# Performance work log

Measured on AMD Instinct MI355X. Metric: run time of the kernel, lower is better.

## Reference

```python
import jax, jax.numpy as jnp
import numpy as np

B = 8192; NP = 20; OBS = 17; ACT = 6; H = 256; N = B * NP
ACT_LIMIT = 1.0; SIGMA_P0 = 0.1; STEPS = 10; LR = 0.05
GAMMA = 1.0 / (1e-8 + 2.0 * 2.0 ** 2)  # kernel_sigma = 2.0
A0_TABLE = 5 * B * NP


def _q_net(x, W1, b1, W2, b2, W3, b3):
    h = jax.nn.relu(x @ W1 + b1)
    h = jax.nn.relu(h @ W2 + b2)
    return (h @ W3 + b3)[:, 0]


def _forward(obs, a0_table, q1_W1, q1_b1, q1_W2, q1_b2, q1_W3, q1_b3,
             q2_W1, q2_b1, q2_W2, q2_b2, q2_W3, q2_b3, idx):
    a0 = a0_table[idx]  # [N, ACT]
    eye = jnp.eye(NP, dtype=obs.dtype)

    def q_min(X):
        xi = jnp.concatenate([obs, X], axis=-1)
        return jnp.minimum(
            _q_net(xi, q1_W1, q1_b1, q1_W2, q1_b2, q1_W3, q1_b3),
            _q_net(xi, q2_W1, q2_b1, q2_W2, q2_b2, q2_W3, q2_b3))

    def step(carry, _):
        a, logp = carry
        logq, vjp_fn = jax.vjp(q_min, a)
        score = vjp_fn(jnp.ones_like(logq))[0]  # autograd.grad(log_prob.sum(), X)
        X = a.reshape(B, NP, ACT)
        S = score.reshape(B, NP, ACT)
        diff = X[:, :, None, :] - X[:, None, :, :]   # [B,n,n,d], x_i - x_j
        dist_sq = (diff ** 2).sum(-1)                # [B,n,n]
        K = jnp.exp(-GAMMA * dist_sq)                # K_XX
        K_grad = -2.0 * GAMMA * diff * K[..., None]  # grad_{x_i} K(x_i, x_j)
        phi = (jnp.einsum('bij,bjd->bid', K, S) + K_grad.sum(1)) / NP
        term1 = (K_grad * S[:, None, :, :]).sum(-1).mean(2)
        term2 = -2.0 * GAMMA * ((K_grad.transpose(0, 2, 1, 3) * diff).sum(-1)
                                - NP * (K - eye)).mean(1)
        logp = logp - LR * (term1 + term2)
        a = a + LR * phi.reshape(N, ACT)
        a = jax.lax.stop_gradient(jnp.clip(a, -ACT_LIMIT, ACT_LIMIT))  # clamp + detach
        return (a, logp), None

    a_init = jax.lax.stop_gradient(a0)  # sampler gets a0.detach()
    (a, logp_svgd), _ = jax.lax.scan(
        step, (a_init, jnp.zeros((B, NP), obs.dtype)), None, length=STEPS)
    a = ACT_LIMIT * jnp.tanh(a)  # [N, ACT]
    logp_normal = (-ACT * 0.5 * np.log(2.0 * np.pi * SIGMA_P0)
                   - 0.5 / SIGMA_P0 * (a0 ** 2).sum(-1).reshape(B, NP))
    logp_tanh = -(2.0 * (np.log(2.0) - a - jax.nn.softplus(-2.0 * a))).sum(-1).reshape(B, NP)
    logp_a = (logp_normal + logp_svgd + logp_tanh).mean(-1)  # [B]
    return a, logp_a


def setup_inputs() -> dict:
    key = jax.random.key(0)
    ks = jax.random.split(key, 9)
    def lin(k, i, o):
        return jax.random.normal(k, (i, o), jnp.float32) / np.sqrt(i)
    din = OBS + ACT
    return {
        'obs': jax.random.normal(ks[0], (N, OBS), jnp.float32),
        'a0_table': SIGMA_P0 * jax.random.normal(ks[1], (A0_TABLE, ACT), jnp.float32),
        'q1_W1': lin(ks[2], din, H), 'q1_b1': jnp.zeros((H,), jnp.float32),
        'q1_W2': lin(ks[3], H, H), 'q1_b2': jnp.zeros((H,), jnp.float32),
        'q1_W3': lin(ks[4], H, 1), 'q1_b3': jnp.zeros((1,), jnp.float32),
        'q2_W1': lin(ks[5], din, H), 'q2_b1': jnp.zeros((H,), jnp.float32),
        'q2_W2': lin(ks[6], H, H), 'q2_b2': jnp.zeros((H,), jnp.float32),
        'q2_W3': lin(ks[7], H, 1), 'q2_b3': jnp.zeros((1,), jnp.float32),
        'idx': jax.random.randint(ks[8], (N,), 0, A0_TABLE),
    }


def reference(obs, a0_table, q1_W1, q1_b1, q1_W2, q1_b2, q1_W3, q1_b3,
              q2_W1, q2_b1, q2_W2, q2_b2, q2_W3, q2_b3, idx):
    return _forward(obs, a0_table, q1_W1, q1_b1, q1_W2, q1_b2, q1_W3, q1_b3,
                    q2_W1, q2_b1, q2_W2, q2_b2, q2_W3, q2_b3, idx)
```

## Files before the change

kernel.cpp:

```cpp
#include <hip/hip_runtime.h>
#include <math.h>

typedef __attribute__((ext_vector_type(8))) __bf16 bf8;
typedef __attribute__((ext_vector_type(4))) __bf16 b4v;
typedef __attribute__((ext_vector_type(4))) float f4;

namespace {
constexpr int kB   = 8192;
constexpr int kNP  = 20;
constexpr int kOBS = 17;
constexpr int kACT = 6;
constexpr int kDIN = 23;
constexpr int kH   = 256;
constexpr int kN   = kB * kNP;
constexpr int BM   = 128;
constexpr int NB   = 8;
constexpr int STR  = 264;
constexpr int XSTR = 40;
constexpr float kLR  = 0.05f;
constexpr float kGAM = (float)(1.0 / (1e-8 + 8.0));
constexpr int PACKN = 8192 + 65536 + 65536 + 4096;
}

__device__ __forceinline__ short f2bf(float f) {
  unsigned u = __builtin_bit_cast(unsigned, f);
  u = (u + 0x7FFFu + ((u >> 16) & 1u)) >> 16;
  return (short)u;
}

__device__ __forceinline__ void lbar() {
  asm volatile("s_waitcnt lgkmcnt(0)" ::: "memory");
  __builtin_amdgcn_s_barrier();
  __builtin_amdgcn_sched_barrier(0);
}

__global__ __launch_bounds__(256) void init_kernel(
    const float* __restrict__ a0_table, const int* __restrict__ idx,
    float* __restrict__ a_buf, float* __restrict__ logp_buf,
    float* __restrict__ a0sq_buf)
{
  int n = blockIdx.x * blockDim.x + threadIdx.x;
  if (n >= kN) return;
  int id = idx[n];
  const float* src = a0_table + (size_t)id * kACT;
  float s = 0.f;
  #pragma unroll
  for (int d = 0; d < kACT; ++d) {
    float v = src[d];
    a_buf[(size_t)n * kACT + d] = v;
    s += v * v;
  }
  a0sq_buf[n] = s;
  logp_buf[n] = 0.f;
}

__global__ __launch_bounds__(256) void pack_kernel(
    const float* __restrict__ W1, const float* __restrict__ b1,
    const float* __restrict__ W2, const float* __restrict__ W3,
    short* __restrict__ out)
{
  int i = blockIdx.x * blockDim.x + threadIdx.x;
  if (i >= PACKN) return;
  float v;
  if (i < 8192) {
    int t = i;
    int j = t & 7, l = (t >> 3) & 63, n = t >> 9;
    int k = ((l >> 4) << 3) + j, c = (n << 4) + (l & 15);
    v = (k < kDIN) ? W1[k * kH + c] : ((k == kDIN) ? b1[c] : 0.f);
  } else if (i < 8192 + 65536) {
    int t = i - 8192;
    int j = t & 7, l = (t >> 3) & 63, nk = t >> 9;
    int n = nk & 15, kk = nk >> 4;
    int k = (kk << 5) + ((l >> 4) << 3) + j, c = (n << 4) + (l & 15);
    v = W2[k * kH + c];
  } else if (i < 8192 + 2 * 65536) {
    int t = i - 8192 - 65536;
    int j = t & 7, l = (t >> 3) & 63, nk = t >> 9;
    int n = nk & 15, kk = nk >> 4;
    int k = (kk << 5) + ((l >> 4) << 3) + j, c = (n << 4) + (l & 15);
    v = W2[c * kH + k] * W3[k];
  } else {
    int t = i - 8192 - 2 * 65536;
    int j = t & 7, l = (t >> 3) & 63, kk = t >> 9;
    int k = (kk << 5) + ((l >> 4) << 3) + j, d = l & 15;
    v = (d < kACT) ? W1[(kOBS + d) * kH + k] : 0.f;
  }
  out[i] = f2bf(v);
}

__global__ __launch_bounds__(512) void score_mfma(
    const float* __restrict__ obs, const float* __restrict__ a_buf,
    const short* __restrict__ pack0, const short* __restrict__ pack1,
    const float* __restrict__ b2a, const float* __restrict__ W3a, const float* __restrict__ b3a,
    const float* __restrict__ b2b, const float* __restrict__ W3b, const float* __restrict__ b3b,
    float* __restrict__ score)
{
  __shared__ __align__(16) __bf16 hbuf[BM * STR];
  __shared__ float qred[8][BM];
  __shared__ float qv_s[2][BM];
  __shared__ float sres[2][BM][8];
  __bf16* xbuf = &hbuf[0];

  const int tid  = threadIdx.x;
  const int wave = tid >> 6, lane = tid & 63;
  const int g16  = lane >> 4, r15 = lane & 15;
  const int wn   = 2 * wave;
  const int swz  = r15 & 8;
  const size_t grow0 = (size_t)blockIdx.x * BM;

  const short* packs[2] = {pack0, pack1};
  const float* b2s[2] = {b2a, b2b};
  const float* W3s[2] = {W3a, W3b};
  const float* b3s[2] = {b3a, b3b};

  const f4 fz = {0.f, 0.f, 0.f, 0.f};
  const __bf16 one_h = (__bf16)1.0f;
  const __bf16 zero_h = (__bf16)0.0f;

#define MM(A, B, C) __builtin_amdgcn_mfma_f32_16x16x32_bf16(A, B, C, 0, 0, 0)
#define AF(nb_, kk_) (*(const bf8*)&hbuf[((nb_) * 16 + r15) * STR + (((kk_) * 32 + g16 * 8) ^ swz)])
#define HW64(nb_, mh_) (*(b4v*)&hbuf[((nb_) * 16 + r15) * STR + ((((wn + (mh_)) * 16) + g16 * 4) ^ swz)])

  #pragma unroll 1
  for (int net = 0; net < 2; ++net) {
    const short* W1p  = packs[net];
    const short* W2p  = W1p + 8192;
    const short* W2Tp = W2p + 65536;
    const short* Wpp  = W2Tp + 65536;
    const float* b2 = b2s[net];
    const float* W3 = W3s[net];
    const float* b3 = b3s[net];

    for (int i = tid; i < BM * 32; i += 512) {
      int r = i >> 5, k = i & 31;
      size_t gr = grow0 + r;
      float v = (k < kOBS) ? obs[gr * kOBS + k]
              : ((k < kDIN) ? a_buf[gr * kACT + (k - kOBS)]
              : ((k == kDIN) ? 1.f : 0.f));
      xbuf[r * XSTR + k] = (__bf16)v;
    }
    lbar();

    bf8 xa[NB];
    #pragma unroll
    for (int nb = 0; nb < NB; ++nb)
      xa[nb] = *(const bf8*)&xbuf[(nb * 16 + r15) * XSTR + g16 * 8];
    lbar();

    f4 acc[NB][2];

    {
      bf8 aw0 = *(const bf8*)&W1p[((wn + 0) * 64 + lane) * 8];
      bf8 aw1 = *(const bf8*)&W1p[((wn + 1) * 64 + lane) * 8];
      __builtin_amdgcn_s_setprio(1);
      #pragma unroll
      for (int nb = 0; nb < NB; ++nb) {
        acc[nb][0] = MM(aw0, xa[nb], fz);
        acc[nb][1] = MM(aw1, xa[nb], fz);
      }
      __builtin_amdgcn_s_setprio(0);
    }

    unsigned m1[NB];
    #pragma unroll
    for (int nb = 0; nb < NB; ++nb) m1[nb] = 0u;
    #pragma unroll
    for (int nb = 0; nb < NB; ++nb) {
      #pragma unroll
      for (int mh = 0; mh < 2; ++mh) {
        b4v w;
        #pragma unroll
        for (int rr = 0; rr < 4; ++rr) {
          float h = acc[nb][mh][rr];
          if (h > 0.f) m1[nb] |= (1u << (mh * 4 + rr));
          w[rr] = (__bf16)fmaxf(h, 0.f);
        }
        HW64(nb, mh) = w;
      }
    }
    float4 b2f[2], w3f[2];
    #pragma unroll
    for (int mh = 0; mh < 2; ++mh) {
      b2f[mh] = *(const float4*)&b2[(wn + mh) * 16 + g16 * 4];
      w3f[mh] = *(const float4*)&W3[(wn + mh) * 16 + g16 * 4];
    }
    lbar();

    {
      bf8 aw0 = *(const bf8*)&W2p[((wn + 0) * 64 + lane) * 8];
      bf8 aw1 = *(const bf8*)&W2p[((wn + 1) * 64 + lane) * 8];
      __builtin_amdgcn_s_setprio(1);
      #pragma unroll
      for (int nb = 0; nb < NB; ++nb) {
        bf8 af = AF(nb, 0);
        acc[nb][0] = MM(aw0, af, fz);
        acc[nb][1] = MM(aw1, af, fz);
      }
      __builtin_amdgcn_s_setprio(0);
    }
    #pragma unroll 2
    for (int kk = 1; kk < 8; ++kk) {
      bf8 aw0 = *(const bf8*)&W2p[((kk * 16 + wn + 0) * 64 + lane) * 8];
      bf8 aw1 = *(const bf8*)&W2p[((kk * 16 + wn + 1) * 64 + lane) * 8];
      __builtin_amdgcn_s_setprio(1);
      #pragma unroll
      for (int nb = 0; nb < NB; ++nb) {
        bf8 af = AF(nb, kk);
        acc[nb][0] = MM(aw0, af, acc[nb][0]);
        acc[nb][1] = MM(aw1, af, acc[nb][1]);
      }
      __builtin_amdgcn_s_setprio(0);
    }
    lbar();

    #pragma unroll
    for (int nb = 0; nb < NB; ++nb) {
      float qn = 0.f;
      #pragma unroll
      for (int mh = 0; mh < 2; ++mh) {
        b4v w;
        #pragma unroll
        for (int rr = 0; rr < 4; ++rr) {
          float h2 = acc[nb][mh][rr] + b2f[mh][rr];
          bool p = h2 > 0.f;
          qn = fmaf(h2, p ? w3f[mh][rr] : 0.f, qn);
          w[rr] = p ? one_h : zero_h;
        }
        HW64(nb, mh) = w;
      }
      qn += __shfl_xor(qn, 16, 64);
      qn += __shfl_xor(qn, 32, 64);
      if (g16 == 0) qred[wave][nb * 16 + r15] = qn;
    }
    lbar();
    if (tid < BM) {
      float q = b3[0];
      #pragma unroll
      for (int w = 0; w < 8; ++w) q += qred[w][tid];
      qv_s[net][tid] = q;
    }

    {
      bf8 aw0 = *(const bf8*)&W2Tp[((wn + 0) * 64 + lane) * 8];
      bf8 aw1 = *(const bf8*)&W2Tp[((wn + 1) * 64 + lane) * 8];
      __builtin_amdgcn_s_setprio(1);
      #pragma unroll
      for (int nb = 0; nb < NB; ++nb) {
        bf8 af = AF(nb, 0);
        acc[nb][0] = MM(aw0, af, fz);
        acc[nb][1] = MM(aw1, af, fz);
      }
      __builtin_amdgcn_s_setprio(0);
    }
    #pragma unroll 2
    for (int kk = 1; kk < 8; ++kk) {
      bf8 aw0 = *(const bf8*)&W2Tp[((kk * 16 + wn + 0) * 64 + lane) * 8];
      bf8 aw1 = *(const bf8*)&W2Tp[((kk * 16 + wn + 1) * 64 + lane) * 8];
      __builtin_amdgcn_s_setprio(1);
      #pragma unroll
      for (int nb = 0; nb < NB; ++nb) {
        bf8 af = AF(nb, kk);
        acc[nb][0] = MM(aw0, af, acc[nb][0]);
        acc[nb][1] = MM(aw1, af, acc[nb][1]);
      }
      __builtin_amdgcn_s_setprio(0);
    }
    lbar();

    #pragma unroll
    for (int nb = 0; nb < NB; ++nb) {
      #pragma unroll
      for (int mh = 0; mh < 2; ++mh) {
        b4v w;
        #pragma unroll
        for (int rr = 0; rr < 4; ++rr)
          w[rr] = ((m1[nb] >> (mh * 4 + rr)) & 1u) ? (__bf16)acc[nb][mh][rr] : zero_h;
        HW64(nb, mh) = w;
      }
    }
    lbar();

    {
      f4 s = fz;
      __builtin_amdgcn_s_setprio(1);
      #pragma unroll
      for (int kk = 0; kk < 8; ++kk) {
        bf8 aw = *(const bf8*)&Wpp[(kk * 64 + lane) * 8];
        bf8 af = AF(wave, kk);
        s = MM(aw, af, s);
      }
      __builtin_amdgcn_s_setprio(0);
      if (g16 < 2) {
        #pragma unroll
        for (int rr = 0; rr < 4; ++rr) {
          int d = g16 * 4 + rr;
          if (d < kACT) sres[net][wave * 16 + r15][d] = s[rr];
        }
      }
    }
    lbar();
  }

  {
    int r = tid >> 2, d4 = tid & 3;
    int sel = (qv_s[0][r] <= qv_s[1][r]) ? 0 : 1;
    #pragma unroll
    for (int pass = 0; pass < 2; ++pass) {
      int d = d4 + pass * 4;
      if (d < kACT)
        score[(grow0 + r) * kACT + d] = sres[sel][r][d];
    }
  }
#undef MM
#undef AF
#undef HW64
}

__global__ __launch_bounds__(256) void svgd_kernel(
    float* __restrict__ a_buf, const float* __restrict__ score,
    float* __restrict__ logp_buf)
{
  __shared__ float X_s[8 * kNP * kACT];
  __shared__ float S_s[8 * kNP * kACT];
  const int tid = threadIdx.x;
  const size_t base = (size_t)blockIdx.x * 8 * kNP * kACT;
  for (int i = tid; i < 8 * kNP * kACT; i += 256) {
    X_s[i] = a_buf[base + i];
    S_s[i] = score[base + i];
  }
  __syncthreads();
  const int g = tid >> 5, p = tid & 31;
  if (p < kNP) {
    const float* X = X_s + g * kNP * kACT;
    const float* S = S_s + g * kNP * kACT;
    float xp[kACT], phi[kACT];
    #pragma unroll
    for (int d = 0; d < kACT; ++d) { xp[d] = X[p * kACT + d]; phi[d] = 0.f; }
    float t1 = 0.f, t2 = 0.f;
    #pragma unroll 1
    for (int q = 0; q < kNP; ++q) {
      float diff[kACT], d2 = 0.f, dot = 0.f;
      #pragma unroll
      for (int d = 0; d < kACT; ++d) {
        float dd = xp[d] - X[q * kACT + d];
        diff[d] = dd; d2 += dd * dd; dot += dd * S[q * kACT + d];
      }
      float Kv = expf(-kGAM * d2);
      #pragma unroll
      for (int d = 0; d < kACT; ++d)
        phi[d] += Kv * S[q * kACT + d] + 2.f * kGAM * diff[d] * Kv;
      t1 += Kv * dot;
      t2 += 2.f * kGAM * d2 * Kv - (float)kNP * (Kv - (q == p ? 1.f : 0.f));
    }
    size_t n = (size_t)blockIdx.x * 8 * kNP + (size_t)g * kNP + p;
    float term12 = (-2.f * kGAM / (float)kNP) * (t1 + t2);
    logp_buf[n] = logp_buf[n] - kLR * term12;
    #pragma unroll
    for (int d = 0; d < kACT; ++d) {
      float na = xp[d] + kLR * (phi[d] * (1.f / (float)kNP));
      na = fminf(fmaxf(na, -1.f), 1.f);
      a_buf[n * kACT + d] = na;
    }
  }
}

__global__ __launch_bounds__(256) void final_kernel(
    const float* __restrict__ a_buf, const float* __restrict__ logp_buf,
    const float* __restrict__ a0sq_buf, float* __restrict__ out_a,
    float* __restrict__ out_logp)
{
  const int tid = threadIdx.x;
  const int g = tid >> 5, p = tid & 31;
  const int b = blockIdx.x * 8 + g;
  float lp = 0.f;
  if (p < kNP) {
    size_t n = (size_t)b * kNP + p;
    float lt = 0.f;
    #pragma unroll
    for (int d = 0; d < kACT; ++d) {
      float a = a_buf[n * kACT + d];
      out_a[n * kACT + d] = tanhf(a);
      lt += 2.f * (0.6931471805599453f - a - log1pf(expf(-2.f * a)));
    }
    float lpn = 1.3941240797541021f - 5.f * a0sq_buf[n];
    lp = lpn + logp_buf[n] - lt;
  }
  #pragma unroll
  for (int m = 16; m >= 1; m >>= 1) lp += __shfl_xor(lp, m, 32);
  if (p == 0) out_logp[b] = lp * (1.f / (float)kNP);
}

extern "C" void kernel_launch(void* const* d_in, const int* in_sizes, int n_in,
                              void* d_out, int out_size, void* d_ws, size_t ws_size,
                              hipStream_t stream)
{
  const float* obs  = (const float*)d_in[0];
  const float* a0t  = (const float*)d_in[1];
  const float* q1W1 = (const float*)d_in[2];
  const float* q1b1 = (const float*)d_in[3];
  const float* q1W2 = (const float*)d_in[4];
  const float* q1b2 = (const float*)d_in[5];
  const float* q1W3 = (const float*)d_in[6];
  const float* q1b3 = (const float*)d_in[7];
  const float* q2W1 = (const float*)d_in[8];
  const float* q2b1 = (const float*)d_in[9];
  const float* q2W2 = (const float*)d_in[10];
  const float* q2b2 = (const float*)d_in[11];
  const float* q2W3 = (const float*)d_in[12];
  const float* q2b3 = (const float*)d_in[13];
  const int*   idx  = (const int*)d_in[14];

  float* a_buf   = (float*)d_ws;
  float* score_b = a_buf   + (size_t)kN * kACT;
  float* logp_b  = score_b + (size_t)kN * kACT;
  float* a0sq_b  = logp_b  + kN;
  short* pack0   = (short*)(a0sq_b + kN);
  short* pack1   = pack0 + PACKN;

  float* out_a  = (float*)d_out;
  float* out_lp = out_a + (size_t)kN * kACT;

  init_kernel<<<(kN + 255) / 256, 256, 0, stream>>>(a0t, idx, a_buf, logp_b, a0sq_b);
  pack_kernel<<<(PACKN + 255) / 256, 256, 0, stream>>>(q1W1, q1b1, q1W2, q1W3, pack0);
  pack_kernel<<<(PACKN + 255) / 256, 256, 0, stream>>>(q2W1, q2b1, q2W2, q2W3, pack1);

  for (int t = 0; t < 10; ++t) {
    score_mfma<<<kN / BM, 512, 0, stream>>>(obs, a_buf, pack0, pack1,
        q1b2, q1W3, q1b3, q2b2, q2W3, q2b3, score_b);
    svgd_kernel<<<kB / 8, 256, 0, stream>>>(a_buf, score_b, logp_b);
  }

  final_kernel<<<kB / 8, 256, 0, stream>>>(a_buf, logp_b, a0sq_b, out_a, out_lp);
}
```

Before: 1.498 ms.

## Fuse SVGD particle update into next step's score kernel with ping-pong buffers

The SVGD update for step t-1 now runs at the start of the score kernel for step t. Each block loads the particle batches overlapping its 128 rows, computes the new actions and logp, and feeds the updated actions straight into its MLP input. Actions and scores ping-pong between two buffers, and scores are stored in bf16. This drops nine separate SVGD launches and one global round trip of actions and scores per step. In exchange, the update runs on only 128 threads before the MFMA work begins, some batches are reloaded by neighbouring blocks, and the bf16 scores add rounding error.

```diff
diff --git a/kernel.cpp b/kernel.cpp
--- a/kernel.cpp
+++ b/kernel.cpp
@@ -30,6 +30,12 @@
 
 __device__ __forceinline__ void lbar() {
   asm volatile("s_waitcnt lgkmcnt(0)" ::: "memory");
+  __builtin_amdgcn_s_barrier();
+  __builtin_amdgcn_sched_barrier(0);
+}
+
+__device__ __forceinline__ void hbar() {
+  asm volatile("s_waitcnt vmcnt(0) lgkmcnt(0)" ::: "memory");
   __builtin_amdgcn_s_barrier();
   __builtin_amdgcn_sched_barrier(0);
 }
@@ -89,11 +95,14 @@
 }
 
 __global__ __launch_bounds__(512) void score_mfma(
-    const float* __restrict__ obs, const float* __restrict__ a_buf,
+    int step,
+    const float* __restrict__ obs,
+    const float* __restrict__ a_prev, float* __restrict__ a_next,
     const short* __restrict__ pack0, const short* __restrict__ pack1,
     const float* __restrict__ b2a, const float* __restrict__ W3a, const float* __restrict__ b3a,
     const float* __restrict__ b2b, const float* __restrict__ W3b, const float* __restrict__ b3b,
-    float* __restrict__ score)
+    const __bf16* __restrict__ s_prev, __bf16* __restrict__ s_out,
+    float* __restrict__ logp_buf)
 {
   __shared__ __align__(16) __bf16 hbuf[BM * STR];
   __shared__ float qred[8][BM];
@@ -120,6 +129,56 @@
 #define MM(A, B, C) __builtin_amdgcn_mfma_f32_16x16x32_bf16(A, B, C, 0, 0, 0)
 #define AF(nb_, kk_) (*(const bf8*)&hbuf[((nb_) * 16 + r15) * STR + (((kk_) * 32 + g16 * 8) ^ swz)])
 #define HW64(nb_, mh_) (*(b4v*)&hbuf[((nb_) * 16 + r15) * STR + ((((wn + (mh_)) * 16) + g16 * 4) ^ swz)])
+
+  float anew[kACT];
+  if (step > 0) {
+    float* Xs = (float*)&hbuf[0];
+    float* Ss = Xs + 160 * kACT;
+    const int b_lo = (int)(grow0 / kNP);
+    const int r_lo = b_lo * kNP;
+    const int b_hi = (int)((grow0 + BM - 1) / kNP);
+    const int nel  = ((b_hi + 1) * kNP - r_lo) * kACT;
+    for (int i = tid; i < nel; i += 512) {
+      Xs[i] = a_prev[(size_t)r_lo * kACT + i];
+      Ss[i] = (float)s_prev[(size_t)r_lo * kACT + i];
+    }
+    lbar();
+    if (tid < BM) {
+      int r = (int)grow0 + tid;
+      int b = r / kNP, p = r - b * kNP;
+      const float* X = Xs + (b - b_lo) * kNP * kACT;
+      const float* S = Ss + (b - b_lo) * kNP * kACT;
+      float xp[kACT], phi[kACT];
+      #pragma unroll
+      for (int d = 0; d < kACT; ++d) { xp[d] = X[p * kACT + d]; phi[d] = 0.f; }
+      float t1 = 0.f, t2 = 0.f;
+      #pragma unroll 1
+      for (int q = 0; q < kNP; ++q) {
+        float diff[kACT], d2 = 0.f, dot = 0.f;
+        #pragma unroll
+        for (int d = 0; d < kACT; ++d) {
+          float dd = xp[d] - X[q * kACT + d];
+          diff[d] = dd; d2 += dd * dd; dot += dd * S[q * kACT + d];
+        }
+        float Kv = expf(-kGAM * d2);
+        #pragma unroll
+        for (int d = 0; d < kACT; ++d)
+          phi[d] += Kv * S[q * kACT + d] + 2.f * kGAM * diff[d] * Kv;
+        t1 += Kv * dot;
+        t2 += 2.f * kGAM * d2 * Kv - (float)kNP * (Kv - (q == p ? 1.f : 0.f));
+      }
+      float term12 = (-2.f * kGAM / (float)kNP) * (t1 + t2);
+      logp_buf[r] = logp_buf[r] - kLR * term12;
+      #pragma unroll
+      for (int d = 0; d < kACT; ++d) {
+        float na = xp[d] + kLR * (phi[d] * (1.f / (float)kNP));
+        na = fminf(fmaxf(na, -1.f), 1.f);
+        anew[d] = na;
+        a_next[(size_t)r * kACT + d] = na;
+      }
+    }
+    hbar();
+  }
 
   #pragma unroll 1
   for (int net = 0; net < 2; ++net) {
@@ -131,13 +190,30 @@
     const float* W3 = W3s[net];
     const float* b3 = b3s[net];
 
-    for (int i = tid; i < BM * 32; i += 512) {
-      int r = i >> 5, k = i & 31;
-      size_t gr = grow0 + r;
-      float v = (k < kOBS) ? obs[gr * kOBS + k]
-              : ((k < kDIN) ? a_buf[gr * kACT + (k - kOBS)]
-              : ((k == kDIN) ? 1.f : 0.f));
-      xbuf[r * XSTR + k] = (__bf16)v;
+    if (step == 0 || net == 1) {
+      const float* asrc = (step == 0) ? a_prev : a_next;
+      for (int i = tid; i < BM * 32; i += 512) {
+        int r = i >> 5, k = i & 31;
+        size_t gr = grow0 + r;
+        float v = (k < kOBS) ? obs[gr * kOBS + k]
+                : ((k < kDIN) ? asrc[gr * kACT + (k - kOBS)]
+                : ((k == kDIN) ? 1.f : 0.f));
+        xbuf[r * XSTR + k] = (__bf16)v;
+      }
+    } else {
+      for (int i = tid; i < BM * 32; i += 512) {
+        int r = i >> 5, k = i & 31;
+        if (k < kOBS) {
+          xbuf[r * XSTR + k] = (__bf16)obs[(grow0 + r) * (size_t)kOBS + k];
+        } else if (k >= kDIN) {
+          xbuf[r * XSTR + k] = (k == kDIN) ? one_h : zero_h;
+        }
+      }
+      if (tid < BM) {
+        #pragma unroll
+        for (int d = 0; d < kACT; ++d)
+          xbuf[tid * XSTR + kOBS + d] = (__bf16)anew[d];
+      }
     }
     lbar();
 
@@ -308,7 +384,7 @@
     for (int pass = 0; pass < 2; ++pass) {
       int d = d4 + pass * 4;
       if (d < kACT)
-        score[(grow0 + r) * kACT + d] = sres[sel][r][d];
+        s_out[(grow0 + r) * kACT + d] = (__bf16)sres[sel][r][d];
     }
   }
 #undef MM
@@ -317,16 +393,16 @@
 }
 
 __global__ __launch_bounds__(256) void svgd_kernel(
-    float* __restrict__ a_buf, const float* __restrict__ score,
-    float* __restrict__ logp_buf)
+    const float* __restrict__ a_in, float* __restrict__ a_out,
+    const __bf16* __restrict__ score, float* __restrict__ logp_buf)
 {
   __shared__ float X_s[8 * kNP * kACT];
   __shared__ float S_s[8 * kNP * kACT];
   const int tid = threadIdx.x;
   const size_t base = (size_t)blockIdx.x * 8 * kNP * kACT;
   for (int i = tid; i < 8 * kNP * kACT; i += 256) {
-    X_s[i] = a_buf[base + i];
-    S_s[i] = score[base + i];
+    X_s[i] = a_in[base + i];
+    S_s[i] = (float)score[base + i];
   }
   __syncthreads();
   const int g = tid >> 5, p = tid & 31;
@@ -359,7 +435,7 @@
     for (int d = 0; d < kACT; ++d) {
       float na = xp[d] + kLR * (phi[d] * (1.f / (float)kNP));
       na = fminf(fmaxf(na, -1.f), 1.f);
-      a_buf[n * kACT + d] = na;
+      a_out[n * kACT + d] = na;
     }
   }
 }
@@ -410,25 +486,31 @@
   const float* q2b3 = (const float*)d_in[13];
   const int*   idx  = (const int*)d_in[14];
 
-  float* a_buf   = (float*)d_ws;
-  float* score_b = a_buf   + (size_t)kN * kACT;
-  float* logp_b  = score_b + (size_t)kN * kACT;
-  float* a0sq_b  = logp_b  + kN;
-  short* pack0   = (short*)(a0sq_b + kN);
-  short* pack1   = pack0 + PACKN;
+  float*  a0buf  = (float*)d_ws;
+  float*  logp_b = a0buf + (size_t)kN * kACT;
+  float*  a0sq_b = logp_b + kN;
+  __bf16* sb0    = (__bf16*)(a0sq_b + kN);
+  __bf16* sb1    = sb0 + (size_t)kN * kACT;
+  short*  pack0  = (short*)(sb1 + (size_t)kN * kACT);
+  short*  pack1  = pack0 + PACKN;
 
   float* out_a  = (float*)d_out;
   float* out_lp = out_a + (size_t)kN * kACT;
 
-  init_kernel<<<(kN + 255) / 256, 256, 0, stream>>>(a0t, idx, a_buf, logp_b, a0sq_b);
+  init_kernel<<<(kN + 255) / 256, 256, 0, stream>>>(a0t, idx, a0buf, logp_b, a0sq_b);
   pack_kernel<<<(PACKN + 255) / 256, 256, 0, stream>>>(q1W1, q1b1, q1W2, q1W3, pack0);
   pack_kernel<<<(PACKN + 255) / 256, 256, 0, stream>>>(q2W1, q2b1, q2W2, q2W3, pack1);
 
   for (int t = 0; t < 10; ++t) {
-    score_mfma<<<kN / BM, 512, 0, stream>>>(obs, a_buf, pack0, pack1,
-        q1b2, q1W3, q1b3, q2b2, q2W3, q2b3, score_b);
-    svgd_kernel<<<kB / 8, 256, 0, stream>>>(a_buf, score_b, logp_b);
-  }
-
-  final_kernel<<<kB / 8, 256, 0, stream>>>(a_buf, logp_b, a0sq_b, out_a, out_lp);
-}
+    const float*  aprev = (t == 0) ? a0buf : (((t - 1) & 1) ? out_a : a0buf);
+    float*        anext = (t & 1) ? out_a : a0buf;
+    const __bf16* sprev = (t & 1) ? sb0 : sb1;
+    __bf16*       sout  = (t & 1) ? sb1 : sb0;
+    score_mfma<<<kN / BM, 512, 0, stream>>>(t, obs, aprev, anext, pack0, pack1,
+        q1b2, q1W3, q1b3, q2b2, q2W3, q2b3, sprev, sout, logp_b);
+  }
+
+  svgd_kernel<<<kB / 8, 256, 0, stream>>>(out_a, a0buf, sb1, logp_b);
+
+  final_kernel<<<kB / 8, 256, 0, stream>>>(a0buf, logp_b, a0sq_b, out_a, out_lp);
+}
```

After: 1.581 ms. 1.06x slower.
